# Kernel tuning notes

Measured on AMD Instinct MI355X. Metric: run time of the kernel, lower is better.

Reference implementation:

```python
import jax, jax.numpy as jnp
import numpy as np

DIM = 128
NUM_HEADS = 8


def setup_inputs() -> dict:
    key = jax.random.key(0)
    ks = jax.random.split(key, 5)
    B, L, C = 4, 16384, DIM
    x = jax.random.normal(ks[0], (B, L, C), dtype=jnp.float32)
    # Linear params (stored as (in, out) so y = x @ W + b)
    w_qkv = jax.random.normal(ks[1], (C, 3 * C), dtype=jnp.float32) * (C ** -0.5)
    b_qkv = jax.random.normal(ks[2], (3 * C,), dtype=jnp.float32) * 0.02
    w_proj = jax.random.normal(ks[3], (C, C), dtype=jnp.float32) * (C ** -0.5)
    b_proj = jax.random.normal(ks[4], (C,), dtype=jnp.float32) * 0.02
    return {"x": x, "w_qkv": w_qkv, "b_qkv": b_qkv, "w_proj": w_proj, "b_proj": b_proj}


def reference(x, w_qkv, b_qkv, w_proj, b_proj):
    B, L, C = x.shape
    H = NUM_HEADS
    hd = C // H
    scale = C ** -0.5  # note: torch code scales by dim**-0.5, not head_dim**-0.5

    qkv = x @ w_qkv + b_qkv                      # (B, L, 3C)
    q, k, v = jnp.split(qkv, 3, axis=-1)         # each (B, L, C)

    def to_heads(t):
        return t.reshape(B, L, H, hd).transpose(0, 2, 1, 3)  # (B, H, L, hd)

    q, k, v = to_heads(q), to_heads(k), to_heads(v)

    # Per-token outer product over head_dim: (B, H, L, hd, hd)
    attn = (q * scale)[..., :, None] * k[..., None, :]
    attn = jax.nn.softmax(attn, axis=-1)

    # attn @ v per token: (B, H, L, hd)
    out = jnp.einsum("bhlij,bhlj->bhli", attn, v)
    out = out.transpose(0, 2, 1, 3).reshape(B, L, C)  # (B, L, C)
    return out @ w_proj + b_proj
```

## Files before the change

kernel.cpp:

```cpp
#include <hip/hip_runtime.h>


typedef __attribute__((ext_vector_type(8))) short bf16x8;
typedef __attribute__((ext_vector_type(4))) float f32x4;
typedef __attribute__((ext_vector_type(4))) unsigned int u32x4;

#define TILE_M 32
#define HALF_M 16
#define QKV_STRIDE_F 388
#define O_STRIDE 136

__device__ __forceinline__ unsigned short f2bf(float f) {
    unsigned int u = __builtin_bit_cast(unsigned int, f);
    u += 0x8000u;
    return (unsigned short)(u >> 16);
}
__device__ __forceinline__ unsigned int pkbf(float lo, float hi) {
    unsigned int a = __builtin_bit_cast(unsigned int, lo) + 0x8000u;
    unsigned int b = __builtin_bit_cast(unsigned int, hi) + 0x8000u;
    return __builtin_amdgcn_perm(b, a, 0x07060302u);
}

__global__ void prep_weights(const float* __restrict__ wqkv,
                             const float* __restrict__ wproj,
                             unsigned short* __restrict__ wqkvT,
                             unsigned short* __restrict__ wprojT) {
    int idx = blockIdx.x * 256 + threadIdx.x;
    if (idx < 384 * 128) {
        int n = idx >> 7, k = idx & 127;
        wqkvT[idx] = f2bf(wqkv[k * 384 + n]);
    }
    if (idx < 128 * 128) {
        int n = idx >> 7, k = idx & 127;
        wprojT[idx] = f2bf(wproj[k * 128 + n]);
    }
}

__global__ __launch_bounds__(256, 4) void fused_channel_attn(
    const float* __restrict__ x,
    const unsigned short* __restrict__ wqkvT,
    const float* __restrict__ bqkv,
    const unsigned short* __restrict__ wprojT,
    const float* __restrict__ bproj,
    float* __restrict__ out)
{
    __shared__ __align__(16) float us_f[HALF_M * QKV_STRIDE_F];
    __shared__ __align__(16) unsigned short us_o[TILE_M * O_STRIDE];

    const int tid  = threadIdx.x;
    const int lane = tid & 63;
    const int wave = tid >> 6;
    const int col  = lane & 15;
    const int quad = lane >> 4;
    const long base_tok = (long)blockIdx.x * TILE_M;

    int ntile[6];
    ntile[0] = 2 * wave;      ntile[1] = 2 * wave + 1;
    ntile[2] = 8 + 2 * wave;  ntile[3] = 9 + 2 * wave;
    ntile[4] = 16 + 2 * wave; ntile[5] = 17 + 2 * wave;

    bf16x8 afr[2][4];
#pragma unroll
    for (int m = 0; m < 2; ++m) {
        const float* xrow = x + (base_tok + m * 16 + col) * 128;
#pragma unroll
        for (int ks = 0; ks < 4; ++ks) {
            const float4* p = (const float4*)(xrow + ks * 32 + quad * 8);
            float4 f0 = p[0], f1 = p[1];
            u32x4 a = {pkbf(f0.x, f0.y), pkbf(f0.z, f0.w),
                       pkbf(f1.x, f1.y), pkbf(f1.z, f1.w)};
            afr[m][ks] = __builtin_bit_cast(bf16x8, a);
        }
    }

    f32x4 acc[2][6];
#pragma unroll
    for (int j = 0; j < 6; ++j) {
        float b = bqkv[ntile[j] * 16 + col];
        acc[0][j] = (f32x4){b, b, b, b};
        acc[1][j] = (f32x4){b, b, b, b};
    }
#pragma unroll
    for (int ks = 0; ks < 4; ++ks) {
        bf16x8 bfr[6];
#pragma unroll
        for (int j = 0; j < 6; ++j)
            bfr[j] = *(const bf16x8*)&wqkvT[(ntile[j] * 16 + col) * 128 + ks * 32 + quad * 8];
#pragma unroll
        for (int j = 0; j < 6; ++j) {
            acc[0][j] = __builtin_amdgcn_mfma_f32_16x16x32_bf16(afr[0][ks], bfr[j], acc[0][j], 0, 0, 0);
            acc[1][j] = __builtin_amdgcn_mfma_f32_16x16x32_bf16(afr[1][ks], bfr[j], acc[1][j], 0, 0, 0);
        }
    }

    const int t    = lane & 15;
    const int hbit = (lane >> 4) & 1;
    const int ih   = lane >> 5;
    const int h    = 2 * wave + hbit;
    const float* qkvrow = us_f + t * QKV_STRIDE_F + h * 16;
    const float sl2e = 0.08838834764831845f * 1.44269504088896340f;

    auto write_qkv_half = [&](int m) {
#pragma unroll
        for (int j = 0; j < 6; ++j)
#pragma unroll
            for (int r = 0; r < 4; ++r)
                us_f[(quad * 4 + r) * QKV_STRIDE_F + ntile[j] * 16 + col] = acc[m][j][r];
    };

    float4 qv4[2], kv4[4], vv4[4];
    auto read_half = [&]() {
        qv4[0] = ((const float4*)(qkvrow + ih * 8))[0];
        qv4[1] = ((const float4*)(qkvrow + ih * 8))[1];
#pragma unroll
        for (int c = 0; c < 4; ++c) {
            kv4[c] = ((const float4*)(qkvrow + 128))[c];
            vv4[c] = ((const float4*)(qkvrow + 256))[c];
        }
    };

    auto compute_attn = [&](int mhalf) {
        float qv[8], kf[16], vf[16];
#pragma unroll
        for (int c = 0; c < 2; ++c) {
            qv[4*c] = qv4[c].x; qv[4*c+1] = qv4[c].y; qv[4*c+2] = qv4[c].z; qv[4*c+3] = qv4[c].w;
        }
#pragma unroll
        for (int c = 0; c < 4; ++c) {
            kf[4*c] = kv4[c].x; kf[4*c+1] = kv4[c].y; kf[4*c+2] = kv4[c].z; kf[4*c+3] = kv4[c].w;
            vf[4*c] = vv4[c].x; vf[4*c+1] = vv4[c].y; vf[4*c+2] = vv4[c].z; vf[4*c+3] = vv4[c].w;
        }
        float ov[8];
#pragma unroll
        for (int i = 0; i < 8; ++i) {
            float qs = qv[i] * sl2e;
            float den = 0.f, num = 0.f;
#pragma unroll
            for (int j = 0; j < 16; ++j) {
                float e = __builtin_amdgcn_exp2f(qs * kf[j]);
                den += e;
                num = fmaf(e, vf[j], num);
            }
            ov[i] = num * __builtin_amdgcn_rcpf(den);
        }
        u32x4 o0 = {pkbf(ov[0], ov[1]), pkbf(ov[2], ov[3]),
                    pkbf(ov[4], ov[5]), pkbf(ov[6], ov[7])};
        *(u32x4*)&us_o[(mhalf * 16 + t) * O_STRIDE + h * 16 + ih * 8] = o0;
    };

    write_qkv_half(0);
    read_half();
    write_qkv_half(1);
    compute_attn(0);
    read_half();
    compute_attn(1);

    __syncthreads();

    const int nb2 = wave * 2;
#pragma unroll
    for (int m = 0; m < 2; ++m) {
        bf16x8 af[4];
#pragma unroll
        for (int ks = 0; ks < 4; ++ks)
            af[ks] = *(const bf16x8*)&us_o[(m * 16 + col) * O_STRIDE + ks * 32 + quad * 8];
        f32x4 acc2[2];
#pragma unroll
        for (int n = 0; n < 2; ++n) {
            float b = bproj[(nb2 + n) * 16 + col];
            acc2[n] = (f32x4){b, b, b, b};
        }
#pragma unroll
        for (int ks = 0; ks < 4; ++ks) {
            bf16x8 bb[2];
#pragma unroll
            for (int n = 0; n < 2; ++n)
                bb[n] = *(const bf16x8*)&wprojT[((nb2 + n) * 16 + col) * 128 + ks * 32 + quad * 8];
#pragma unroll
            for (int n = 0; n < 2; ++n)
                acc2[n] = __builtin_amdgcn_mfma_f32_16x16x32_bf16(af[ks], bb[n], acc2[n], 0, 0, 0);
        }
#pragma unroll
        for (int n = 0; n < 2; ++n)
#pragma unroll
            for (int r = 0; r < 4; ++r) {
                long tt = base_tok + m * 16 + quad * 4 + r;
                out[tt * 128 + (nb2 + n) * 16 + col] = acc2[n][r];
            }
    }
}

extern "C" void kernel_launch(void* const* d_in, const int* in_sizes, int n_in,
                              void* d_out, int out_size, void* d_ws, size_t ws_size,
                              hipStream_t stream) {
    const float* x     = (const float*)d_in[0];
    const float* wqkv  = (const float*)d_in[1];
    const float* bqkv  = (const float*)d_in[2];
    const float* wproj = (const float*)d_in[3];
    const float* bproj = (const float*)d_in[4];
    float* out = (float*)d_out;

    unsigned short* wqkvT  = (unsigned short*)d_ws;
    unsigned short* wprojT = wqkvT + 384 * 128;

    prep_weights<<<192, 256, 0, stream>>>(wqkv, wproj, wqkvT, wprojT);

    const int tokens = in_sizes[0] / 128;
    fused_channel_attn<<<tokens / TILE_M, 256, 0, stream>>>(
        x, wqkvT, bqkv, wprojT, bproj, out);
}
```

Baseline: 129.6 us.

## Process two token tiles per block and prefetch next tile's x during attention

Each block now handles two consecutive 32-token tiles, which halves the grid. While the attention math for the first tile runs, the x loads for the second tile are issued and packed to bf16, hiding global-load latency behind the exp-heavy compute. The second tile's QKV MFMA runs before the first tile's projection. This raises register pressure through the prefetch buffers, and the smaller grid (1024 blocks) may reduce occupancy or load balance across CUs.

Measured after the change: 139.6 us. 1.08x slower.

```diff
diff --git a/kernel.cpp b/kernel.cpp
--- a/kernel.cpp
+++ b/kernel.cpp
@@ -52,46 +52,55 @@
     const int wave = tid >> 6;
     const int col  = lane & 15;
     const int quad = lane >> 4;
-    const long base_tok = (long)blockIdx.x * TILE_M;
+    const long tok0 = (long)blockIdx.x * 2 * TILE_M;
+    const long tok1 = tok0 + TILE_M;
 
     int ntile[6];
     ntile[0] = 2 * wave;      ntile[1] = 2 * wave + 1;
     ntile[2] = 8 + 2 * wave;  ntile[3] = 9 + 2 * wave;
     ntile[4] = 16 + 2 * wave; ntile[5] = 17 + 2 * wave;
 
+    float bqv[6];
+#pragma unroll
+    for (int j = 0; j < 6; ++j) bqv[j] = bqkv[ntile[j] * 16 + col];
+
     bf16x8 afr[2][4];
-#pragma unroll
-    for (int m = 0; m < 2; ++m) {
-        const float* xrow = x + (base_tok + m * 16 + col) * 128;
+    f32x4  acc[2][6];
+
+    auto load_pack_x = [&](long bt) {
+#pragma unroll
+        for (int m = 0; m < 2; ++m) {
+            const float* xrow = x + (bt + m * 16 + col) * 128;
+#pragma unroll
+            for (int ks = 0; ks < 4; ++ks) {
+                const float4* p = (const float4*)(xrow + ks * 32 + quad * 8);
+                float4 f0 = p[0], f1 = p[1];
+                u32x4 a = {pkbf(f0.x, f0.y), pkbf(f0.z, f0.w),
+                           pkbf(f1.x, f1.y), pkbf(f1.z, f1.w)};
+                afr[m][ks] = __builtin_bit_cast(bf16x8, a);
+            }
+        }
+    };
+
+    auto mfma_qkv = [&]() {
+#pragma unroll
+        for (int j = 0; j < 6; ++j) {
+            acc[0][j] = (f32x4){bqv[j], bqv[j], bqv[j], bqv[j]};
+            acc[1][j] = (f32x4){bqv[j], bqv[j], bqv[j], bqv[j]};
+        }
 #pragma unroll
         for (int ks = 0; ks < 4; ++ks) {
-            const float4* p = (const float4*)(xrow + ks * 32 + quad * 8);
-            float4 f0 = p[0], f1 = p[1];
-            u32x4 a = {pkbf(f0.x, f0.y), pkbf(f0.z, f0.w),
-                       pkbf(f1.x, f1.y), pkbf(f1.z, f1.w)};
-            afr[m][ks] = __builtin_bit_cast(bf16x8, a);
-        }
-    }
-
-    f32x4 acc[2][6];
-#pragma unroll
-    for (int j = 0; j < 6; ++j) {
-        float b = bqkv[ntile[j] * 16 + col];
-        acc[0][j] = (f32x4){b, b, b, b};
-        acc[1][j] = (f32x4){b, b, b, b};
-    }
-#pragma unroll
-    for (int ks = 0; ks < 4; ++ks) {
-        bf16x8 bfr[6];
-#pragma unroll
-        for (int j = 0; j < 6; ++j)
-            bfr[j] = *(const bf16x8*)&wqkvT[(ntile[j] * 16 + col) * 128 + ks * 32 + quad * 8];
-#pragma unroll
-        for (int j = 0; j < 6; ++j) {
-            acc[0][j] = __builtin_amdgcn_mfma_f32_16x16x32_bf16(afr[0][ks], bfr[j], acc[0][j], 0, 0, 0);
-            acc[1][j] = __builtin_amdgcn_mfma_f32_16x16x32_bf16(afr[1][ks], bfr[j], acc[1][j], 0, 0, 0);
-        }
-    }
+            bf16x8 bfr[6];
+#pragma unroll
+            for (int j = 0; j < 6; ++j)
+                bfr[j] = *(const bf16x8*)&wqkvT[(ntile[j] * 16 + col) * 128 + ks * 32 + quad * 8];
+#pragma unroll
+            for (int j = 0; j < 6; ++j) {
+                acc[0][j] = __builtin_amdgcn_mfma_f32_16x16x32_bf16(afr[0][ks], bfr[j], acc[0][j], 0, 0, 0);
+                acc[1][j] = __builtin_amdgcn_mfma_f32_16x16x32_bf16(afr[1][ks], bfr[j], acc[1][j], 0, 0, 0);
+            }
+        }
+    };
 
     const int t    = lane & 15;
     const int hbit = (lane >> 4) & 1;
@@ -100,7 +109,7 @@
     const float* qkvrow = us_f + t * QKV_STRIDE_F + h * 16;
     const float sl2e = 0.08838834764831845f * 1.44269504088896340f;
 
-    auto write_qkv_half = [&](int m) {
+    auto write_half = [&](int m) {
 #pragma unroll
         for (int j = 0; j < 6; ++j)
 #pragma unroll
@@ -119,7 +128,7 @@
         }
     };
 
-    auto compute_attn = [&](int mhalf) {
+    auto attn_half = [&](int mhalf) {
         float qv[8], kf[16], vf[16];
 #pragma unroll
         for (int c = 0; c < 2; ++c) {
@@ -148,46 +157,99 @@
         *(u32x4*)&us_o[(mhalf * 16 + t) * O_STRIDE + h * 16 + ih * 8] = o0;
     };
 
-    write_qkv_half(0);
-    read_half();
-    write_qkv_half(1);
-    compute_attn(0);
-    read_half();
-    compute_attn(1);
+    auto stage_c = [&](long bt) {
+        const int nb2 = wave * 2;
+#pragma unroll
+        for (int m = 0; m < 2; ++m) {
+            bf16x8 af[4];
+#pragma unroll
+            for (int ks = 0; ks < 4; ++ks)
+                af[ks] = *(const bf16x8*)&us_o[(m * 16 + col) * O_STRIDE + ks * 32 + quad * 8];
+            f32x4 acc2[2];
+#pragma unroll
+            for (int n = 0; n < 2; ++n) {
+                float b = bproj[(nb2 + n) * 16 + col];
+                acc2[n] = (f32x4){b, b, b, b};
+            }
+#pragma unroll
+            for (int ks = 0; ks < 4; ++ks) {
+                bf16x8 bb[2];
+#pragma unroll
+                for (int n = 0; n < 2; ++n)
+                    bb[n] = *(const bf16x8*)&wprojT[((nb2 + n) * 16 + col) * 128 + ks * 32 + quad * 8];
+#pragma unroll
+                for (int n = 0; n < 2; ++n)
+                    acc2[n] = __builtin_amdgcn_mfma_f32_16x16x32_bf16(af[ks], bb[n], acc2[n], 0, 0, 0);
+            }
+#pragma unroll
+            for (int n = 0; n < 2; ++n)
+#pragma unroll
+                for (int r = 0; r < 4; ++r) {
+                    long tt = bt + m * 16 + quad * 4 + r;
+                    out[tt * 128 + (nb2 + n) * 16 + col] = acc2[n][r];
+                }
+        }
+    };
+
+    load_pack_x(tok0);
+    mfma_qkv();
+
+    write_half(0);
+    read_half();
+
+    float4 xp[8];
+    {
+        const float* xrow = x + (tok1 + col) * 128;
+#pragma unroll
+        for (int ks = 0; ks < 4; ++ks) {
+            const float4* p = (const float4*)(xrow + ks * 32 + quad * 8);
+            xp[2*ks] = p[0]; xp[2*ks+1] = p[1];
+        }
+    }
+    write_half(1);
+    attn_half(0);
+
+#pragma unroll
+    for (int ks = 0; ks < 4; ++ks) {
+        float4 f0 = xp[2*ks], f1 = xp[2*ks+1];
+        u32x4 a = {pkbf(f0.x, f0.y), pkbf(f0.z, f0.w),
+                   pkbf(f1.x, f1.y), pkbf(f1.z, f1.w)};
+        afr[0][ks] = __builtin_bit_cast(bf16x8, a);
+    }
+    {
+        const float* xrow = x + (tok1 + 16 + col) * 128;
+#pragma unroll
+        for (int ks = 0; ks < 4; ++ks) {
+            const float4* p = (const float4*)(xrow + ks * 32 + quad * 8);
+            xp[2*ks] = p[0]; xp[2*ks+1] = p[1];
+        }
+    }
+    read_half();
+    attn_half(1);
+#pragma unroll
+    for (int ks = 0; ks < 4; ++ks) {
+        float4 f0 = xp[2*ks], f1 = xp[2*ks+1];
+        u32x4 a = {pkbf(f0.x, f0.y), pkbf(f0.z, f0.w),
+                   pkbf(f1.x, f1.y), pkbf(f1.z, f1.w)};
+        afr[1][ks] = __builtin_bit_cast(bf16x8, a);
+    }
 
     __syncthreads();
 
-    const int nb2 = wave * 2;
-#pragma unroll
-    for (int m = 0; m < 2; ++m) {
-        bf16x8 af[4];
-#pragma unroll
-        for (int ks = 0; ks < 4; ++ks)
-            af[ks] = *(const bf16x8*)&us_o[(m * 16 + col) * O_STRIDE + ks * 32 + quad * 8];
-        f32x4 acc2[2];
-#pragma unroll
-        for (int n = 0; n < 2; ++n) {
-            float b = bproj[(nb2 + n) * 16 + col];
-            acc2[n] = (f32x4){b, b, b, b};
-        }
-#pragma unroll
-        for (int ks = 0; ks < 4; ++ks) {
-            bf16x8 bb[2];
-#pragma unroll
-            for (int n = 0; n < 2; ++n)
-                bb[n] = *(const bf16x8*)&wprojT[((nb2 + n) * 16 + col) * 128 + ks * 32 + quad * 8];
-#pragma unroll
-            for (int n = 0; n < 2; ++n)
-                acc2[n] = __builtin_amdgcn_mfma_f32_16x16x32_bf16(af[ks], bb[n], acc2[n], 0, 0, 0);
-        }
-#pragma unroll
-        for (int n = 0; n < 2; ++n)
-#pragma unroll
-            for (int r = 0; r < 4; ++r) {
-                long tt = base_tok + m * 16 + quad * 4 + r;
-                out[tt * 128 + (nb2 + n) * 16 + col] = acc2[n][r];
-            }
-    }
+    mfma_qkv();
+    stage_c(tok0);
+
+    __syncthreads();
+
+    write_half(0);
+    read_half();
+    write_half(1);
+    attn_half(0);
+    read_half();
+    attn_half(1);
+
+    __syncthreads();
+    stage_c(tok1);
 }
 
 extern "C" void kernel_launch(void* const* d_in, const int* in_sizes, int n_in,
@@ -206,6 +268,6 @@
     prep_weights<<<192, 256, 0, stream>>>(wqkv, wproj, wqkvT, wprojT);
 
     const int tokens = in_sizes[0] / 128;
-    fused_channel_attn<<<tokens / TILE_M, 256, 0, stream>>>(
+    fused_channel_attn<<<tokens / (2 * TILE_M), 256, 0, stream>>>(
         x, wqkvT, bqkv, wprojT, bproj, out);
 }
```
